# Optimization experiments

Hardware: AMD Instinct MI355X
Metric: run time of the kernel (lower is better)

Reference implementation:

```python
import jax, jax.numpy as jnp
import numpy as np

KS, ST, PD = 4, 2, 1
AZI = 2.0 * np.pi / 1024.0
INC = 0.0073
C_IN, C_OUT = 64, 128


def _buffers():
    # torch: cos_azi[sh, sw] = cos(azi * (sw - ks//2)); cos_inc[sh, sw] = cos(inc * (sh - ks//2))
    d = np.arange(KS, dtype=np.float32) - KS // 2
    cos_azi = np.broadcast_to(np.cos(AZI * d)[None, :], (KS, KS))
    sin_azi = np.broadcast_to(np.sin(AZI * d)[None, :], (KS, KS))
    cos_inc = np.broadcast_to(np.cos(INC * d)[:, None], (KS, KS))
    sin_inc = np.broadcast_to(np.sin(INC * d)[:, None], (KS, KS))
    shp = (1, 1, 1, 1, KS, KS)
    return tuple(jnp.asarray(np.ascontiguousarray(b).reshape(shp), jnp.float32)
                 for b in (cos_azi, sin_azi, cos_inc, sin_inc))


def _pad(a, w_value):
    # pad width with constant, then height circularly (matches F.pad order in torch code)
    a = jnp.pad(a, ((0, 0), (0, 0), (0, 0), (PD, PD)), constant_values=w_value)
    return jnp.pad(a, ((0, 0), (0, 0), (PD, PD), (0, 0)), mode='wrap')


def _unfold(a):
    # torch a.unfold(3, ks, st).unfold(2, ks, st) -> [B,C,Ho,Wo,kw,kh]
    B, C, Hp, Wp = a.shape
    Ho = (Hp - KS) // ST + 1
    Wo = (Wp - KS) // ST + 1
    ih = (ST * jnp.arange(Ho))[:, None] + jnp.arange(KS)  # [Ho, ks]
    iw = (ST * jnp.arange(Wo))[:, None] + jnp.arange(KS)  # [Wo, ks]
    p = a[:, :, ih[:, None, :, None], iw[None, :, None, :]]  # [B,C,Ho,Wo,kh,kw]
    return jnp.transpose(p, (0, 1, 2, 3, 5, 4))               # [B,C,Ho,Wo,kw,kh]


def _forward(x, r, W1, b1, W2, b2, Wc, bc):
    cos_azi, sin_azi, cos_inc, sin_inc = _buffers()
    rp = _unfold(_pad(r, 100.0))                      # [B,1,Ho,Wo,kw,kh]
    r_center = rp[:, :, :, :, KS // 2, KS // 2]       # [B,1,Ho,Wo]
    pe0 = rp * cos_azi * cos_inc - r_center[..., None, None]
    pe1 = rp * cos_azi * sin_inc
    pe2 = rp * sin_azi
    pe = jnp.concatenate([pe0, pe1, pe2], axis=1)     # [B,3,Ho,Wo,kw,kh]
    pe = jnp.transpose(pe, (0, 2, 3, 4, 5, 1))        # [B,Ho,Wo,kw,kh,3]
    h = jax.nn.leaky_relu(pe @ W1 + b1, 0.2)          # [B,Ho,Wo,kw,kh,C]
    w = h @ W2 + b2                                   # [B,Ho,Wo,kw,kh,C]
    w = jnp.transpose(w, (0, 5, 1, 2, 3, 4))          # [B,C,Ho,Wo,kw,kh]
    xp = _unfold(_pad(x, 0.0)) * w                    # [B,C,Ho,Wo,kw,kh]
    B, C, Ho, Wo = xp.shape[:4]
    xp = jnp.transpose(xp, (0, 1, 4, 5, 2, 3)).reshape(B, C * KS * KS, Ho, Wo)
    out = jnp.einsum('bkhw,ok->bohw', xp, Wc) + bc[None, :, None, None]
    return out, r_center


def setup_inputs() -> dict:
    key = jax.random.key(0)
    ks = jax.random.split(key, 8)
    B, H, W = 4, 64, 1024
    x = jax.random.normal(ks[0], (B, C_IN, H, W), jnp.float32)
    r = jax.random.uniform(ks[1], (B, 1, H, W), jnp.float32) * 50.0  # metres
    W1 = jax.random.normal(ks[2], (3, C_IN), jnp.float32) * 0.3
    b1 = jax.random.normal(ks[3], (C_IN,), jnp.float32) * 0.02
    W2 = jax.random.normal(ks[4], (C_IN, C_IN), jnp.float32) * (1.0 / np.sqrt(C_IN))
    b2 = jax.random.normal(ks[5], (C_IN,), jnp.float32) * 0.02
    Wc = jax.random.normal(ks[6], (C_OUT, C_IN * KS * KS), jnp.float32) * (1.0 / np.sqrt(C_IN * KS * KS))
    bc = jax.random.normal(ks[7], (C_OUT,), jnp.float32) * 0.02
    return {'x': x, 'r': r, 'W1': W1, 'b1': b1, 'W2': W2, 'b2': b2, 'Wc': Wc, 'bc': bc}


def reference(x, r, W1, b1, W2, b2, Wc, bc):
    return _forward(x, r, W1, b1, W2, b2, Wc, bc)
```

## Files before the change

### kernel.cpp

```cpp
#include <hip/hip_runtime.h>
#include <hip/hip_bf16.h>

namespace {

constexpr int B_   = 4;
constexpr int CIN  = 64;
constexpr int COUT = 128;
constexpr int HIN  = 64,  WIN  = 1024;
constexpr int HOUT = 32,  WOUT = 512;
constexpr int TW   = 16;
constexpr int SP   = 1096;
constexpr int KTOT = CIN * 16;

typedef __bf16 bf16x8 __attribute__((ext_vector_type(8)));
typedef float  f32x4  __attribute__((ext_vector_type(4)));

__global__ void cvt_wts(const float* __restrict__ Wc, const float* __restrict__ W2,
                        __hip_bfloat16* __restrict__ wcb, __hip_bfloat16* __restrict__ w2t) {
    int i = blockIdx.x * 256 + threadIdx.x;
    if (i < COUT * KTOT) {
        int o = i >> 10, k = i & 1023, tap = k >> 6, c = k & 63;
        wcb[i] = __float2bfloat16(Wc[(size_t)o * KTOT + c * 16 + tap]);
    } else if (i < COUT * KTOT + CIN * CIN) {
        int m = i - COUT * KTOT;
        int c = m >> 6, c1 = m & 63;
        w2t[m] = __float2bfloat16(W2[c1 * CIN + c]);
    }
}

__global__ __launch_bounds__(256, 3)
void fused_ccconv(const float* __restrict__ x,  const float* __restrict__ r,
                  const float* __restrict__ W1, const float* __restrict__ b1,
                  const __hip_bfloat16* __restrict__ W2T, const float* __restrict__ b2,
                  const __hip_bfloat16* __restrict__ WcB, const float* __restrict__ bc,
                  float* __restrict__ out)
{
    __shared__ __hip_bfloat16 S[TW * SP];

    const int t   = threadIdx.x;
    const int bx  = blockIdx.x;
    const int wt  = bx & 31;
    const int ho  = (bx >> 5) & 31;
    const int b   = bx >> 10;
    const int wo0 = wt * TW;

    const float* rb = r + (size_t)b * HIN * WIN;

    if (t < TW) {
        const int wo = wo0 + t;
        out[(size_t)B_*COUT*HOUT*WOUT + ((size_t)b*HOUT + ho)*WOUT + wo] =
            rb[(2*ho + 1)*WIN + (2*wo + 1)];
    }

    const int ln   = t & 63;
    const int wv   = t >> 6;
    const int lm   = ln & 15;
    const int quad = ln >> 4;

    const float AZI = 0.006135923151542565f;
    const float INC = 0.0073f;

    {
        bf16x8 bfr[4][2];
        float  b2v[4];
        #pragma unroll
        for (int nt = 0; nt < 4; ++nt) {
            #pragma unroll
            for (int ks = 0; ks < 2; ++ks)
                bfr[nt][ks] = *reinterpret_cast<const bf16x8*>(
                    W2T + (nt*16 + lm)*CIN + ks*32 + quad*8);
            b2v[nt] = b2[nt*16 + lm];
        }

        const int i_ = lm >> 2, j_ = lm & 3;
        const float di = (float)(i_ - 2), dj = (float)(j_ - 2);
        const float cA = cosf(AZI * dj), sA = sinf(AZI * dj);
        const float cI = cosf(INC * di), sI = sinf(INC * di);
        const int hsrc = (2*ho + j_ + 63) & 63;

        #pragma unroll
        for (int mt = 0; mt < 4; ++mt) {
            const int p  = wv*4 + mt;
            const int wo = wo0 + p;
            const int wsrc = 2*wo + i_ - 1;
            const bool inb = (unsigned)wsrc < (unsigned)WIN;
            const float rpv = inb ? rb[hsrc*WIN + wsrc] : 100.0f;
            const float rc  = rb[(2*ho + 1)*WIN + (2*wo + 1)];
            const float pe0 = rpv * cA * cI - rc;
            const float pe1 = rpv * cA * sI;
            const float pe2 = rpv * sA;

            bf16x8 af0, af1;
            #pragma unroll
            for (int ks = 0; ks < 2; ++ks) {
                const int cb = ks*32 + quad*8;
                #pragma unroll
                for (int j = 0; j < 8; ++j) {
                    const int c1 = cb + j;
                    float hv = fmaf(pe0, W1[c1],
                               fmaf(pe1, W1[CIN + c1],
                               fmaf(pe2, W1[2*CIN + c1], b1[c1])));
                    hv = (hv >= 0.0f) ? hv : 0.2f * hv;
                    __hip_bfloat16 hb = __float2bfloat16(hv);
                    if (ks == 0) af0[j] = *reinterpret_cast<__bf16*>(&hb);
                    else         af1[j] = *reinterpret_cast<__bf16*>(&hb);
                }
            }

            #pragma unroll
            for (int nt = 0; nt < 4; ++nt) {
                f32x4 acc = {b2v[nt], b2v[nt], b2v[nt], b2v[nt]};
                acc = __builtin_amdgcn_mfma_f32_16x16x32_bf16(af0, bfr[nt][0], acc, 0, 0, 0);
                acc = __builtin_amdgcn_mfma_f32_16x16x32_bf16(af1, bfr[nt][1], acc, 0, 0, 0);
                #pragma unroll
                for (int q = 0; q < 4; ++q)
                    S[p*SP + (quad*4 + q)*68 + nt*16 + lm] = __float2bfloat16(acc[q]);
            }
        }
    }

    {
        const int p   = t >> 4;
        const int tap = t & 15;
        const int i_  = tap >> 2, j_ = tap & 3;
        const int hsrc = (2*ho + j_ + 63) & 63;
        const int wo   = wo0 + p;
        const int wsrc = 2*wo + i_ - 1;
        const bool inb = (unsigned)wsrc < (unsigned)WIN;

        uint2 wrow[16];
        const uint2* wp = reinterpret_cast<const uint2*>(S + p*SP + tap*68);
        #pragma unroll
        for (int u = 0; u < 16; ++u) wrow[u] = wp[u];

        const float* xb = x + (size_t)b*CIN*HIN*WIN + hsrc*WIN + wsrc;

        float xall[CIN];
        #pragma unroll
        for (int c = 0; c < CIN; ++c)
            xall[c] = inb ? xb[(size_t)c * HIN * WIN] : 0.0f;

        uint4* Ap = reinterpret_cast<uint4*>(S + p*SP + tap*64);
        #pragma unroll
        for (int g = 0; g < 8; ++g) {
            uint pk[4];
            #pragma unroll
            for (int pr = 0; pr < 4; ++pr) {
                const int c0 = g*8 + pr*2;
                const uint2 wv2 = wrow[c0 >> 2];
                const uint word = (c0 & 2) ? wv2.y : wv2.x;
                const float w0 = __uint_as_float(word << 16);
                const float w1 = __uint_as_float(word & 0xffff0000u);
                __hip_bfloat16 p0 = __float2bfloat16(w0 * xall[c0]);
                __hip_bfloat16 p1 = __float2bfloat16(w1 * xall[c0 + 1]);
                const uint lo = *reinterpret_cast<unsigned short*>(&p0);
                const uint hi = *reinterpret_cast<unsigned short*>(&p1);
                pk[pr] = lo | (hi << 16);
            }
            Ap[g] = make_uint4(pk[0], pk[1], pk[2], pk[3]);
        }
    }

    __syncthreads();

    {
        const int o0 = wv * 32;
        const __hip_bfloat16* wcP0 = WcB + ((size_t)(o0 + lm)) * KTOT + quad*8;
        const __hip_bfloat16* wcP1 = wcP0 + (size_t)16 * KTOT;
        const __hip_bfloat16* aP   = S + lm*SP + quad*8;

        f32x4 acc0 = {0.f,0.f,0.f,0.f};
        f32x4 acc1 = {0.f,0.f,0.f,0.f};

        #pragma unroll 4
        for (int ks = 0; ks < KTOT/32; ++ks) {
            const bf16x8 af = *reinterpret_cast<const bf16x8*>(aP   + ks*32);
            const bf16x8 w0 = *reinterpret_cast<const bf16x8*>(wcP0 + ks*32);
            const bf16x8 w1 = *reinterpret_cast<const bf16x8*>(wcP1 + ks*32);
            acc0 = __builtin_amdgcn_mfma_f32_16x16x32_bf16(w0, af, acc0, 0, 0, 0);
            acc1 = __builtin_amdgcn_mfma_f32_16x16x32_bf16(w1, af, acc1, 0, 0, 0);
        }

        #pragma unroll
        for (int q = 0; q < 4; ++q) {
            const int oa = o0 + quad*4 + q;
            const int ob = oa + 16;
            out[(((size_t)b*COUT + oa)*HOUT + ho)*WOUT + wo0 + lm] = acc0[q] + bc[oa];
            out[(((size_t)b*COUT + ob)*HOUT + ho)*WOUT + wo0 + lm] = acc1[q] + bc[ob];
        }
    }
}

}

extern "C" void kernel_launch(void* const* d_in, const int* in_sizes, int n_in,
                              void* d_out, int out_size, void* d_ws, size_t ws_size,
                              hipStream_t stream) {
    const float* x  = (const float*)d_in[0];
    const float* r  = (const float*)d_in[1];
    const float* W1 = (const float*)d_in[2];
    const float* b1 = (const float*)d_in[3];
    const float* W2 = (const float*)d_in[4];
    const float* b2 = (const float*)d_in[5];
    const float* Wc = (const float*)d_in[6];
    const float* bc = (const float*)d_in[7];
    float* out = (float*)d_out;

    __hip_bfloat16* wcb = (__hip_bfloat16*)d_ws;
    __hip_bfloat16* w2t = (__hip_bfloat16*)((char*)d_ws + 262144);

    const int ntot = COUT*KTOT + CIN*CIN;
    hipLaunchKernelGGL(cvt_wts, dim3((ntot + 255)/256), dim3(256), 0, stream,
                       Wc, W2, wcb, w2t);

    dim3 grid(B_ * HOUT * (WOUT / TW));
    dim3 block(256);
    hipLaunchKernelGGL(fused_ccconv, grid, block, 0, stream,
                       x, r, W1, b1, w2t, b2, wcb, bc, out);
}
```

Before: 290.5 us.

## Prefetch half of x early, swizzle LDS A tile, raise occupancy bound

Issues the global loads for the first 32 input channels of x at kernel start, so they overlap with the W1/W2 MLP phase; the remaining 32 are loaded later. It also applies an XOR swizzle to the LDS layout of the product tile to reduce bank conflicts on the writes and the MFMA reads. Launch bounds rise from 3 to 4 waves per SIMD and the K loop unroll goes from 4 to 8. Holding the prefetched registers across the MLP phase adds register pressure, which conflicts with the higher occupancy target and could cause spills.

```diff
diff --git a/kernel.cpp b/kernel.cpp
--- a/kernel.cpp
+++ b/kernel.cpp
@@ -28,7 +28,7 @@
     }
 }
 
-__global__ __launch_bounds__(256, 3)
+__global__ __launch_bounds__(256, 4)
 void fused_ccconv(const float* __restrict__ x,  const float* __restrict__ r,
                   const float* __restrict__ W1, const float* __restrict__ b1,
                   const __hip_bfloat16* __restrict__ W2T, const float* __restrict__ b2,
@@ -45,6 +45,19 @@
     const int wo0 = wt * TW;
 
     const float* rb = r + (size_t)b * HIN * WIN;
+
+    const int pp    = t >> 4;
+    const int ptap  = t & 15;
+    const int pi    = ptap >> 2, pj = ptap & 3;
+    const int phsrc = (2*ho + pj + 63) & 63;
+    const int pwsrc = 2*(wo0 + pp) + pi - 1;
+    const bool pinb = (unsigned)pwsrc < (unsigned)WIN;
+    const float* xb = x + (size_t)b*CIN*HIN*WIN + phsrc*WIN + pwsrc;
+
+    float xlo[32];
+    #pragma unroll
+    for (int c = 0; c < 32; ++c)
+        xlo[c] = pinb ? xb[(size_t)c * HIN * WIN] : 0.0f;
 
     if (t < TW) {
         const int wo = wo0 + t;
@@ -120,27 +133,19 @@
     }
 
     {
-        const int p   = t >> 4;
-        const int tap = t & 15;
-        const int i_  = tap >> 2, j_ = tap & 3;
-        const int hsrc = (2*ho + j_ + 63) & 63;
-        const int wo   = wo0 + p;
-        const int wsrc = 2*wo + i_ - 1;
-        const bool inb = (unsigned)wsrc < (unsigned)WIN;
+        float xhi[32];
+        #pragma unroll
+        for (int c = 0; c < 32; ++c)
+            xhi[c] = pinb ? xb[(size_t)(c + 32) * HIN * WIN] : 0.0f;
 
         uint2 wrow[16];
-        const uint2* wp = reinterpret_cast<const uint2*>(S + p*SP + tap*68);
+        const uint2* wp = reinterpret_cast<const uint2*>(S + pp*SP + ptap*68);
         #pragma unroll
         for (int u = 0; u < 16; ++u) wrow[u] = wp[u];
 
-        const float* xb = x + (size_t)b*CIN*HIN*WIN + hsrc*WIN + wsrc;
-
-        float xall[CIN];
-        #pragma unroll
-        for (int c = 0; c < CIN; ++c)
-            xall[c] = inb ? xb[(size_t)c * HIN * WIN] : 0.0f;
-
-        uint4* Ap = reinterpret_cast<uint4*>(S + p*SP + tap*64);
+        const int swz = (ptap & 7) << 4;
+        char* Abase = reinterpret_cast<char*>(S + pp*SP) + ptap*128;
+
         #pragma unroll
         for (int g = 0; g < 8; ++g) {
             uint pk[4];
@@ -151,13 +156,16 @@
                 const uint word = (c0 & 2) ? wv2.y : wv2.x;
                 const float w0 = __uint_as_float(word << 16);
                 const float w1 = __uint_as_float(word & 0xffff0000u);
-                __hip_bfloat16 p0 = __float2bfloat16(w0 * xall[c0]);
-                __hip_bfloat16 p1 = __float2bfloat16(w1 * xall[c0 + 1]);
+                const float xv0 = (c0     < 32) ? xlo[c0]        : xhi[c0 - 32];
+                const float xv1 = (c0 + 1 < 32) ? xlo[c0 + 1]    : xhi[c0 - 31];
+                __hip_bfloat16 p0 = __float2bfloat16(w0 * xv0);
+                __hip_bfloat16 p1 = __float2bfloat16(w1 * xv1);
                 const uint lo = *reinterpret_cast<unsigned short*>(&p0);
                 const uint hi = *reinterpret_cast<unsigned short*>(&p1);
                 pk[pr] = lo | (hi << 16);
             }
-            Ap[g] = make_uint4(pk[0], pk[1], pk[2], pk[3]);
+            *reinterpret_cast<uint4*>(Abase + ((g*16) ^ swz)) =
+                make_uint4(pk[0], pk[1], pk[2], pk[3]);
         }
     }
 
@@ -167,14 +175,18 @@
         const int o0 = wv * 32;
         const __hip_bfloat16* wcP0 = WcB + ((size_t)(o0 + lm)) * KTOT + quad*8;
         const __hip_bfloat16* wcP1 = wcP0 + (size_t)16 * KTOT;
-        const __hip_bfloat16* aP   = S + lm*SP + quad*8;
+        const char* aRow = reinterpret_cast<const char*>(S + lm*SP);
+        const int qoff = quad << 4;
 
         f32x4 acc0 = {0.f,0.f,0.f,0.f};
         f32x4 acc1 = {0.f,0.f,0.f,0.f};
 
-        #pragma unroll 4
+        #pragma unroll 8
         for (int ks = 0; ks < KTOT/32; ++ks) {
-            const bf16x8 af = *reinterpret_cast<const bf16x8*>(aP   + ks*32);
+            const int tap = ks >> 1;
+            const int rem = ((ks & 1) << 6) + qoff;
+            const bf16x8 af = *reinterpret_cast<const bf16x8*>(
+                aRow + tap*128 + (rem ^ ((tap & 7) << 4)));
             const bf16x8 w0 = *reinterpret_cast<const bf16x8*>(wcP0 + ks*32);
             const bf16x8 w1 = *reinterpret_cast<const bf16x8*>(wcP1 + ks*32);
             acc0 = __builtin_amdgcn_mfma_f32_16x16x32_bf16(w0, af, acc0, 0, 0, 0);
```

New measurement: 339.0 us. 1.17x slower.
